# Kernel tuning notes

Hardware: AMD Instinct MI355X
Metric: run time of the kernel (lower is better)

## Reference

```python
import jax, jax.numpy as jnp
import numpy as np

B = 1024
D = 128  # in_out_dim


def _lin(k, i, o):
    return jax.random.normal(k, (i, o), jnp.float32) / np.sqrt(i)


def setup_inputs() -> dict:
    key = jax.random.key(0)
    ks = jax.random.split(key, 24)
    inp = {
        'pseudo_t': jax.random.uniform(ks[0], (), jnp.float32),
        'x': jax.random.normal(ks[1], (B, D), jnp.float32),
        'g_x': jax.random.normal(ks[2], (B, 1), jnp.float32),
        'p': jax.random.uniform(ks[3], (B, 1), jnp.float32),
        # GRN encoder: 128->1024->960->896 (Tanh), decoder 896->128
        'gw0': _lin(ks[4], 128, 1024), 'gb0': jnp.zeros((1024,), jnp.float32),
        'gw1': _lin(ks[5], 1024, 960), 'gb1': jnp.zeros((960,), jnp.float32),
        'gw2': _lin(ks[6], 960, 896), 'gb2': jnp.zeros((896,), jnp.float32),
        'gdw': _lin(ks[7], 896, 128), 'gdb': jnp.zeros((128,), jnp.float32),
        # BRD encoder: 129->512->448 (Tanh), decoder 448->1
        'bw0': _lin(ks[8], 129, 512), 'bb0': jnp.zeros((512,), jnp.float32),
        'bw1': _lin(ks[9], 512, 448), 'bb1': jnp.zeros((448,), jnp.float32),
        'bdw': _lin(ks[10], 448, 1), 'bdb': jnp.zeros((1,), jnp.float32),
    }
    return inp


def reference(pseudo_t, x, g_x, p, gw0, gb0, gw1, gb1, gw2, gb2, gdw, gdb,
              bw0, bb0, bw1, bb1, bdw, bdb):
    bsz = x.shape[0]
    x_gene = x[:, :-1]                       # [B, D-1]
    s = jnp.full((bsz, 1), pseudo_t, x.dtype)

    def grn(state):                          # [..., D] -> [..., D]
        h = jnp.tanh(state @ gw0 + gb0)
        h = jnp.tanh(h @ gw1 + gb1)
        h = jnp.tanh(h @ gw2 + gb2)
        return h @ gdw + gdb

    dx_dt = grn(jnp.concatenate([s, x_gene], axis=1))   # [B, D]

    # BRD growth function g(x, t)
    st = jnp.concatenate([s, x], axis=1)                # [B, D+1]
    e = jnp.tanh(st @ bw0 + bb0)
    e = jnp.tanh(e @ bw1 + bb1)
    g = e @ bdw + bdb                                   # [B, 1]

    # trace of d(dx_dt[:, :D-1]) / d(x_gene), per sample (CNF divergence)
    s_scalar = jnp.reshape(pseudo_t, (1,)).astype(x.dtype)

    def f_single(xg_i):                                 # [D-1] -> [D]
        return grn(jnp.concatenate([s_scalar, xg_i]))

    jac = jax.vmap(jax.jacfwd(f_single))(x_gene)        # [B, D, D-1]
    tr = jnp.trace(jac[:, :D - 1, :], axis1=1, axis2=2) # [B]

    dp_dt = g - p * tr[:, None]                         # [B, 1]
    return (dx_dt, g, dp_dt)
```

## Files before the change

### kernel.cpp

```cpp
#include <hip/hip_runtime.h>


typedef __bf16 bf16;
typedef __bf16 bf16x8 __attribute__((ext_vector_type(8)));
typedef float floatx4 __attribute__((ext_vector_type(4)));

#if defined(__has_builtin)
#if __has_builtin(__builtin_amdgcn_global_load_lds)
#define HAVE_GLL 1
#endif
#endif

typedef __attribute__((address_space(3))) char lds_char_t;
typedef __attribute__((address_space(1))) const char gbl_char_t;

__device__ inline void async_load16(const void* gp, void* lp) {
#ifdef HAVE_GLL
  __builtin_amdgcn_global_load_lds((gbl_char_t*)gp, (lds_char_t*)lp, 16, 0, 0);
#else
  *(bf16x8*)lp = *(const bf16x8*)gp;
#endif
}

__device__ inline void stage_async(const bf16* src, long row0, int ld, int kc,
                                   bf16* dst, int wid, int sr8, int cph) {
#pragma unroll
  for (int t = 0; t < 4; ++t) {
    const int r = (wid * 4 + t) * 8 + sr8;
    const int csrc = (cph - r) & 7;
    async_load16(src + (row0 + r) * (size_t)ld + kc + csrc * 8,
                 dst + r * 64 + cph * 8);
  }
}

__device__ inline void mfma_block(const bf16* As, const bf16* Bs,
                                  floatx4 (&acc)[4][4], int wm, int wn,
                                  int l16, int quad) {
#pragma unroll
  for (int ks = 0; ks < 2; ++ks) {
    bf16x8 af[4], bfv[4];
#pragma unroll
    for (int mt = 0; mt < 4; ++mt) {
      const int r = wm * 64 + mt * 16 + l16;
      const int c = (ks * 4 + quad + r) & 7;
      af[mt] = *(const bf16x8*)(As + r * 64 + c * 8);
    }
#pragma unroll
    for (int nt = 0; nt < 4; ++nt) {
      const int r = wn * 64 + nt * 16 + l16;
      const int c = (ks * 4 + quad + r) & 7;
      bfv[nt] = *(const bf16x8*)(Bs + r * 64 + c * 8);
    }
#pragma unroll
    for (int mt = 0; mt < 4; ++mt)
#pragma unroll
      for (int nt = 0; nt < 4; ++nt)
        acc[mt][nt] = __builtin_amdgcn_mfma_f32_16x16x32_bf16(af[mt], bfv[nt], acc[mt][nt], 0, 0, 0);
  }
}

__device__ inline void g0_body(bf16* G0, const bf16* gw0b, const bf16* d0b,
                               int i0, int ch, int b, int tid) {
  const int nb = ((b >> 9) << 3) + (b & 7);
  const int inner = (b >> 3) & 63;
  if (nb >= ch) return;
  const int e = inner * 256 + tid;
  const int d = e >> 7;
  const int j = (e & 127) << 3;
  const int ig = i0 + nb;
  const int wsel = (d + 1 < 128) ? d + 1 : 127;
  bf16x8 gv = *(const bf16x8*)(gw0b + wsel * 1024 + j);
  bf16x8 dv = *(const bf16x8*)(d0b + (size_t)ig * 1024 + j);
  bf16x8 v;
#pragma unroll
  for (int k = 0; k < 8; ++k) v[k] = (bf16)((float)gv[k] * (float)dv[k]);
  *(bf16x8*)(G0 + ((size_t)nb * 128 + d) * 1024 + j) = v;
}

struct T8 {
  const bf16* A;
  const bf16* Bm;
  const bf16* sc;
  bf16* Upr;
  const float* gdw;
  float* tr;
  int i0, NT, ch, nTiles;
  int chn, i0n;
  bf16* G0;
  const bf16* gw0b;
  const bf16* d0b;
};

__device__ __forceinline__ void gemm256(const bf16* Aop, const bf16* Bop,
                                        int m0, int n0, int NT, char* lds,
                                        floatx4 (&acc)[8][4]) {
  const int tid = threadIdx.x;
  const int wid = tid >> 6, lane = tid & 63;
  const int wm = wid & 1, wn = wid >> 1;
  const int quad = lane >> 4, l16 = lane & 15;

  const int sr = tid >> 2;
  const int sg = tid & 3;
  const int csrc = (sg - (sr >> 1)) & 3;
  const bf16* aSrc = Aop + (size_t)(m0 + sr) * 1024 + csrc * 8;
  const bf16* bSrc = Bop + (size_t)(n0 + sr) * 1024 + csrc * 8;

  const int rA = wm * 128 + l16;
  const int rB = wn * 64 + l16;
  const int aOff = rA * 64 + ((quad + (rA >> 1)) & 3) * 16;
  const int bOff = rB * 64 + ((quad + (rB >> 1)) & 3) * 16;

#define STAGE4(hh)                                                             \
  {                                                                            \
    char* db = lds + ((hh) & 3) * 32768;                                       \
    const int kce = (hh) * 32;                                                 \
    async_load16(aSrc + kce, db + tid * 16);                                   \
    async_load16(aSrc + 131072 + kce, db + 8192 + tid * 16);                   \
    async_load16(bSrc + kce, db + 16384 + tid * 16);                           \
    async_load16(bSrc + 131072 + kce, db + 24576 + tid * 16);                  \
  }

#define HALF_COMPUTE(HB)                                                       \
  {                                                                            \
    const char* hb_ = (const char*)(HB);                                       \
    bf16x8 af[8], bv[4];                                                       \
    _Pragma("unroll")                                                          \
    for (int nf = 0; nf < 4; ++nf)                                             \
      bv[nf] = *(const bf16x8*)(hb_ + 16384 + bOff + nf * 1024);               \
    _Pragma("unroll")                                                          \
    for (int mf = 0; mf < 8; ++mf)                                             \
      af[mf] = *(const bf16x8*)(hb_ + aOff + mf * 1024);                       \
    _Pragma("unroll")                                                          \
    for (int mf = 0; mf < 8; ++mf)                                             \
      _Pragma("unroll")                                                        \
      for (int nf = 0; nf < 4; ++nf)                                           \
        acc[mf][nf] = __builtin_amdgcn_mfma_f32_16x16x32_bf16(                 \
            af[mf], bv[nf], acc[mf][nf], 0, 0, 0);                             \
  }

#define VMW(N) asm volatile("s_waitcnt vmcnt(" #N ")" ::: "memory")
#define BARRIER()                                                              \
  asm volatile("s_barrier" ::: "memory");                                      \
  __builtin_amdgcn_sched_barrier(0)

  STAGE4(0);
  STAGE4(1);
  VMW(4);
  BARRIER();

#pragma unroll 2
  for (int t = 0; t < NT; ++t) {
    const int h0 = 2 * t;
    const bool more = (t + 1 < NT);

    if (more) STAGE4(h0 + 2);
    HALF_COMPUTE(lds + (h0 & 3) * 32768);
    if (more) VMW(4); else VMW(0);
    BARRIER();

    if (more) STAGE4(h0 + 3);
    HALF_COMPUTE(lds + ((h0 + 1) & 3) * 32768);
    if (more) {
      VMW(4);
      BARRIER();
    }
  }
#undef STAGE4
#undef HALF_COMPUTE
#undef VMW
#undef BARRIER
}

__global__ __launch_bounds__(512, 2) void kt8_b1(T8 p) {
  extern __shared__ __align__(16) char lds[];
  const int bid = blockIdx.x;
  const int nt  = ((bid >> 4) << 3) | (bid & 7);
  const int mtp = (bid >> 3) & 1;
  if (nt >= p.nTiles) return;

  const int tid = threadIdx.x;
  const int wid = tid >> 6, lane = tid & 63;
  const int wm = wid & 1, wn = wid >> 1;
  const int quad = lane >> 4, l16 = lane & 15;
  const long nLim = (long)p.ch * 128;

#pragma unroll 1
  for (int q = 0; q < 2; ++q) {
    const int mt = mtp * 2 + q;
    floatx4 acc[8][4];
#pragma unroll
    for (int a = 0; a < 8; ++a)
#pragma unroll
      for (int b = 0; b < 4; ++b)
#pragma unroll
        for (int r = 0; r < 4; ++r) acc[a][b][r] = 0.0f;

    gemm256(p.A, p.Bm, mt * 256, nt * 256, p.NT, lds, acc);

    const int mb = mt * 256 + wm * 128;
#pragma unroll
    for (int nf = 0; nf < 4; ++nf) {
      const long n = (long)nt * 256 + wn * 64 + nf * 16 + l16;
      if (n < nLim) {
        const int ig = p.i0 + (int)(n >> 7);
        const bf16* dp = p.sc + (size_t)ig * 960;
        bf16* urow = p.Upr + (size_t)n * 1024;
#pragma unroll
        for (int mf = 0; mf < 8; ++mf) {
          const int mg = mb + mf * 16 + quad * 4;
          if (mg < 960) {
            union { bf16 h[4]; uint2 u; } o;
#pragma unroll
            for (int r = 0; r < 4; ++r)
              o.h[r] = (bf16)(acc[mf][nf][r] * (float)dp[mg + r]);
            *(uint2*)(urow + mg) = o.u;
          }
        }
      }
    }
  }
}

__global__ __launch_bounds__(512, 2) void kt8_b2(T8 p) {
  extern __shared__ __align__(16) char lds[];
  const int bid = blockIdx.x;
  const int nt  = ((bid >> 4) << 3) | (bid & 7);
  const int mtp = (bid >> 3) & 1;
  const int tid = threadIdx.x;

  if (nt < p.nTiles) {
    const int wid = tid >> 6, lane = tid & 63;
    const int wm = wid & 1, wn = wid >> 1;
    const int quad = lane >> 4, l16 = lane & 15;
    const long nLim = (long)p.ch * 128;

    float s = 0.0f;
#pragma unroll 1
    for (int q = 0; q < 2; ++q) {
      const int mt = mtp * 2 + q;
      floatx4 acc[8][4];
#pragma unroll
      for (int a = 0; a < 8; ++a)
#pragma unroll
        for (int b = 0; b < 4; ++b)
#pragma unroll
          for (int r = 0; r < 4; ++r) acc[a][b][r] = 0.0f;

      gemm256(p.A, p.Bm, mt * 256, nt * 256, p.NT, lds, acc);

      const int mb = mt * 256 + wm * 128;
#pragma unroll
      for (int nf = 0; nf < 4; ++nf) {
        const long n = (long)nt * 256 + wn * 64 + nf * 16 + l16;
        const int d = (int)(n & 127);
        if (n < nLim && d < 127) {
          const int ig = p.i0 + (int)(n >> 7);
          const bf16* dp = p.sc + (size_t)ig * 896;
#pragma unroll
          for (int mf = 0; mf < 8; ++mf) {
            const int mg = mb + mf * 16 + quad * 4;
            if (mg < 896) {
#pragma unroll
              for (int r = 0; r < 4; ++r) {
                const float w = (float)dp[mg + r] * p.gdw[(mg + r) * 128 + d];
                s += acc[mf][nf][r] * w;
              }
            }
          }
        }
      }
    }
#pragma unroll
    for (int off = 1; off < 64; off <<= 1) s += __shfl_xor(s, off, 64);
    float* red = (float*)lds;
    if (lane == 0) red[wid] = s;
    __syncthreads();
    const int igA = p.i0 + nt * 2;
    if (tid == 0)
      atomicAdd(p.tr + igA, red[0] + red[1] + red[2] + red[3]);
    if (tid == 256 && nt * 2 + 1 < p.ch)
      atomicAdd(p.tr + igA + 1, red[4] + red[5] + red[6] + red[7]);
  }

  if (p.chn > 0) {
    const size_t V = (size_t)p.chn * 16384;
    for (size_t v = (size_t)blockIdx.x * 512 + tid; v < V;
         v += (size_t)gridDim.x * 512) {
      const int j = ((int)(v & 127)) << 3;
      const size_t rest = v >> 7;
      const int d = (int)(rest & 127);
      const int nb = (int)(rest >> 7);
      const int wsel = (d + 1 < 128) ? d + 1 : 127;
      bf16x8 gv = *(const bf16x8*)(p.gw0b + wsel * 1024 + j);
      bf16x8 dv = *(const bf16x8*)(p.d0b + (size_t)(p.i0n + nb) * 1024 + j);
      bf16x8 o;
#pragma unroll
      for (int k = 0; k < 8; ++k) o[k] = (bf16)((float)gv[k] * (float)dv[k]);
      *(bf16x8*)(p.G0 + ((size_t)nb * 128 + d) * 1024 + j) = o;
    }
  }
}

struct FArgs {
  const bf16* A; int lda;
  const bf16* Bt; int ldb;
  const float* bias;
  bf16* C; int ldc;
  bf16* D; int ldd;
  float* outF; int ldo;
  int K; int realN; int gridX;
};

template <int ACT>
__device__ inline void fwd_body(const FArgs& p, int bx, bf16* As, bf16* Bs) {
  const int tid  = threadIdx.x;
  const int wid  = tid >> 6, lane = tid & 63;
  const int wm   = wid & 1, wn = wid >> 1;
  const int quad = lane >> 4, l16 = lane & 15;
  const int sr8  = lane >> 3, cph = lane & 7;
  const int m0   = (bx % p.gridX) * 128;
  const int bn0  = (bx / p.gridX) * 128;

  floatx4 acc[4][4];
#pragma unroll
  for (int a = 0; a < 4; ++a)
#pragma unroll
    for (int b = 0; b < 4; ++b)
#pragma unroll
      for (int r = 0; r < 4; ++r) acc[a][b][r] = 0.0f;

  for (int kc = 0; kc < p.K; kc += 64) {
    stage_async(p.A, m0, p.lda, kc, As, wid, sr8, cph);
    stage_async(p.Bt, bn0, p.ldb, kc, Bs, wid, sr8, cph);
    __syncthreads();
    mfma_block(As, Bs, acc, wm, wn, l16, quad);
    __syncthreads();
  }

#pragma unroll
  for (int nt = 0; nt < 4; ++nt) {
    const int ng = bn0 + wn * 64 + nt * 16 + l16;
    const float bv = (ng < p.realN) ? p.bias[ng] : 0.0f;
#pragma unroll
    for (int mt = 0; mt < 4; ++mt)
#pragma unroll
      for (int r = 0; r < 4; ++r) {
        const int i = m0 + wm * 64 + mt * 16 + quad * 4 + r;
        const float v = acc[mt][nt][r] + bv;
        if (ACT) {
          const float t = tanhf(v);
          p.C[(size_t)i * p.ldc + ng] = (ng < p.realN) ? (bf16)t : (bf16)0.0f;
          if (p.D && ng < p.realN)
            p.D[(size_t)i * p.ldd + ng] = (bf16)(1.0f - t * t);
        } else if (ng < p.realN) {
          p.outF[(size_t)i * p.ldo + ng] = v;
        }
      }
  }
}

__global__ __launch_bounds__(256) void kt_fwd2(FArgs a, int na, FArgs b) {
  __shared__ __align__(16) bf16 As[8192];
  __shared__ __align__(16) bf16 Bs[8192];
  const int bx = blockIdx.x;
  if (bx < na) fwd_body<1>(a, bx, As, Bs);
  else         fwd_body<1>(b, bx - na, As, Bs);
}

__global__ __launch_bounds__(256) void kt_l2g0(FArgs a, int na, bf16* G0,
                                               const bf16* gw0b, const bf16* d0b,
                                               int i0, int ch) {
  __shared__ __align__(16) bf16 As[8192];
  __shared__ __align__(16) bf16 Bs[8192];
  const int bx = blockIdx.x;
  if (bx < na) fwd_body<1>(a, bx, As, Bs);
  else         g0_body(G0, gw0b, d0b, i0, ch, bx - na, threadIdx.x);
}

__global__ __launch_bounds__(256) void kt_dxgdot(FArgs a, int na,
                                                 const bf16* e1b, const float* bdw,
                                                 const float* bdb, float* gf,
                                                 float* gout) {
  __shared__ __align__(16) bf16 As[8192];
  __shared__ __align__(16) bf16 Bs[8192];
  const int bx = blockIdx.x;
  if (bx < na) { fwd_body<0>(a, bx, As, Bs); return; }
  const int i = (bx - na) * 4 + (threadIdx.x >> 6);
  const int lane = threadIdx.x & 63;
  float s = 0.0f;
  for (int k = lane; k < 448; k += 64) s += (float)e1b[(size_t)i * 512 + k] * bdw[k];
#pragma unroll
  for (int off = 32; off > 0; off >>= 1) s += __shfl_down(s, off, 64);
  if (lane == 0) {
    const float v = s + bdb[0];
    gf[i] = v;
    gout[i] = v;
  }
}

struct PArgs {
  const float *gw0, *gw1, *gw2, *gdw, *bw0, *bw1, *pt, *x;
  bf16 *gw0b, *gw0t, *gw1t, *gw2t, *gdwt, *bw0t, *bw1t, *Xg, *Xb;
};

__device__ inline void tpose_tile(bf16* dst, const float* src, int R, int C,
                                  int ldd, int tile, int tilesX, float* tl,
                                  int tid) {
  const int r0 = (tile % tilesX) * 64;
  const int c0 = (tile / tilesX) * 64;
  const int tx = tid & 63, ty0 = tid >> 6;
#pragma unroll
  for (int i = 0; i < 16; ++i) {
    const int ty = ty0 + i * 4;
    const int r = r0 + ty, c = c0 + tx;
    tl[ty * 65 + tx] = (r < R && c < C) ? src[(size_t)r * C + c] : 0.0f;
  }
  __syncthreads();
#pragma unroll
  for (int i = 0; i < 16; ++i) {
    const int ty = ty0 + i * 4;
    dst[(size_t)(c0 + ty) * ldd + r0 + tx] = (bf16)tl[tx * 65 + ty];
  }
}

__global__ __launch_bounds__(256) void kt_prep(PArgs p) {
  __shared__ float tl[64 * 65];
  int b = blockIdx.x;
  const int t = threadIdx.x;
  if (b < 512) { p.gw0b[b * 256 + t] = (bf16)p.gw0[b * 256 + t]; return; }
  b -= 512;
  if (b < 768) {
    const int idx = b * 256 + t;
    const int i = idx / 192, c = idx % 192;
    const float s = p.pt[0];
    float vb;
    if (c == 0) vb = s;
    else if (c <= 128) vb = p.x[i * 128 + c - 1];
    else vb = 0.0f;
    p.Xb[i * 192 + c] = (bf16)vb;
    if (c < 128) p.Xg[i * 128 + c] = (bf16)((c == 0) ? s : p.x[i * 128 + c - 1]);
    return;
  }
  b -= 768;
  if (b < 32)  { tpose_tile(p.gw0t, p.gw0, 128, 1024, 128, b, 2, tl, t);  return; }
  b -= 32;
  if (b < 256) { tpose_tile(p.gw1t, p.gw1, 1024, 960, 1024, b, 16, tl, t); return; }
  b -= 256;
  if (b < 256) { tpose_tile(p.gw2t, p.gw2, 960, 896, 1024, b, 16, tl, t); return; }
  b -= 256;
  if (b < 32)  { tpose_tile(p.gdwt, p.gdw, 896, 128, 1024, b, 16, tl, t); return; }
  b -= 32;
  if (b < 24)  { tpose_tile(p.bw0t, p.bw0, 129, 512, 192, b, 3, tl, t);  return; }
  b -= 24;
  if (b < 64)  { tpose_tile(p.bw1t, p.bw1, 512, 448, 512, b, 8, tl, t);  return; }
}

__global__ __launch_bounds__(256) void kt_fin(const float* gf, const float* tr,
                                              const float* pp, float* dp) {
  const int i = blockIdx.x * 256 + threadIdx.x;
  if (i < 1024) dp[i] = gf[i] - pp[i] * tr[i];
}

extern "C" void kernel_launch(void* const* d_in, const int* in_sizes, int n_in,
                              void* d_out, int out_size, void* d_ws, size_t ws_size,
                              hipStream_t stream) {
  const float* pt  = (const float*)d_in[0];
  const float* x   = (const float*)d_in[1];
  const float* pp  = (const float*)d_in[3];
  const float* gw0 = (const float*)d_in[4];
  const float* gb0 = (const float*)d_in[5];
  const float* gw1 = (const float*)d_in[6];
  const float* gb1 = (const float*)d_in[7];
  const float* gw2 = (const float*)d_in[8];
  const float* gb2 = (const float*)d_in[9];
  const float* gdw = (const float*)d_in[10];
  const float* gdb = (const float*)d_in[11];
  const float* bw0 = (const float*)d_in[12];
  const float* bb0 = (const float*)d_in[13];
  const float* bw1 = (const float*)d_in[14];
  const float* bb1 = (const float*)d_in[15];
  const float* bdw = (const float*)d_in[16];
  const float* bdb = (const float*)d_in[17];
  float* out = (float*)d_out;

  static bool s_attr = false;
  if (!s_attr) {
    hipFuncSetAttribute((const void*)kt8_b1,
                        hipFuncAttributeMaxDynamicSharedMemorySize, 131072);
    hipFuncSetAttribute((const void*)kt8_b2,
                        hipFuncAttributeMaxDynamicSharedMemorySize, 131072);
    s_attr = true;
  }

  char* w = (char*)d_ws;
  size_t used = 0;
  auto alloc = [&](size_t nbytes) -> void* {
    void* r = w + used;
    used += (nbytes + 255) & ~(size_t)255;
    return r;
  };
  bf16* gw0b = (bf16*)alloc((size_t)128 * 1024 * 2);
  bf16* gw0t = (bf16*)alloc((size_t)1024 * 128 * 2);
  bf16* gw1t = (bf16*)alloc((size_t)1024 * 1024 * 2);
  bf16* gw2t = (bf16*)alloc((size_t)1024 * 1024 * 2);
  bf16* gdwt = (bf16*)alloc((size_t)128 * 1024 * 2);
  bf16* bw0t = (bf16*)alloc((size_t)512 * 192 * 2);
  bf16* bw1t = (bf16*)alloc((size_t)512 * 512 * 2);
  bf16* Xg   = (bf16*)alloc((size_t)1024 * 128 * 2);
  bf16* Xb   = (bf16*)alloc((size_t)1024 * 192 * 2);
  bf16* h0b  = (bf16*)alloc((size_t)1024 * 1024 * 2);
  bf16* h1b  = (bf16*)alloc((size_t)1024 * 1024 * 2);
  bf16* h2b  = (bf16*)alloc((size_t)1024 * 1024 * 2);
  bf16* e0b  = (bf16*)alloc((size_t)1024 * 512 * 2);
  bf16* e1b  = (bf16*)alloc((size_t)1024 * 512 * 2);
  bf16* d0b  = (bf16*)alloc((size_t)1024 * 1024 * 2);
  bf16* d1b  = (bf16*)alloc((size_t)1024 * 960 * 2);
  bf16* d2b  = (bf16*)alloc((size_t)1024 * 896 * 2);
  float* gf  = (float*)alloc(1024 * 4);
  float* tr  = (float*)alloc(1024 * 4);

  const size_t perSample = (size_t)128 * 1024 * 2;
  size_t avail = (ws_size > used) ? ws_size - used : 0;
  int CH = (int)(avail / (2 * perSample));
  if (CH > 256) CH = 256;
  if (CH >= 2) CH &= ~1;
  if (CH < 1) CH = 1;
  bf16* G0  = (bf16*)alloc((size_t)CH * perSample);
  bf16* Upr = (bf16*)(w + used);

  hipMemsetAsync(tr, 0, 1024 * 4, stream);

  {
    PArgs a{gw0, gw1, gw2, gdw, bw0, bw1, pt, x,
            gw0b, gw0t, gw1t, gw2t, gdwt, bw0t, bw1t, Xg, Xb};
    kt_prep<<<dim3(1944), 256, 0, stream>>>(a);
  }

  {
    FArgs a{}; a.A = Xg; a.lda = 128; a.Bt = gw0t; a.ldb = 128; a.bias = gb0;
    a.C = h0b; a.ldc = 1024; a.D = d0b; a.ldd = 1024; a.K = 128; a.realN = 1024;
    a.gridX = 8;
    FArgs b{}; b.A = Xb; b.lda = 192; b.Bt = bw0t; b.ldb = 192; b.bias = bb0;
    b.C = e0b; b.ldc = 512; b.K = 192; b.realN = 512; b.gridX = 8;
    kt_fwd2<<<dim3(96), 256, 0, stream>>>(a, 64, b);
  }
  {
    FArgs a{}; a.A = h0b; a.lda = 1024; a.Bt = gw1t; a.ldb = 1024; a.bias = gb1;
    a.C = h1b; a.ldc = 1024; a.D = d1b; a.ldd = 960; a.K = 1024; a.realN = 960;
    a.gridX = 8;
    FArgs b{}; b.A = e0b; b.lda = 512; b.Bt = bw1t; b.ldb = 512; b.bias = bb1;
    b.C = e1b; b.ldc = 512; b.K = 512; b.realN = 448; b.gridX = 8;
    kt_fwd2<<<dim3(96), 256, 0, stream>>>(a, 64, b);
  }
  const int ch0  = (1024 < CH) ? 1024 : CH;
  const int ch08 = (ch0 + 7) & ~7;
  {
    FArgs a{}; a.A = h1b; a.lda = 1024; a.Bt = gw2t; a.ldb = 1024; a.bias = gb2;
    a.C = h2b; a.ldc = 1024; a.D = d2b; a.ldd = 896; a.K = 1024; a.realN = 896;
    a.gridX = 8;
    kt_l2g0<<<dim3(56 + ch08 * 64), 256, 0, stream>>>(a, 56, G0, gw0b, d0b, 0, ch0);
  }
  {
    FArgs a{}; a.A = h2b; a.lda = 1024; a.Bt = gdwt; a.ldb = 1024; a.bias = gdb;
    a.outF = out; a.ldo = 128; a.K = 896; a.realN = 128; a.gridX = 8;
    kt_dxgdot<<<dim3(8 + 256), 256, 0, stream>>>(a, 8, e1b, bdw, bdb, gf, out + 131072);
  }

  for (int i0 = 0; i0 < 1024; i0 += CH) {
    const int ch  = (1024 - i0 < CH) ? (1024 - i0) : CH;
    const int nTiles = (ch * 128 + 255) >> 8;
    const int nT8 = (nTiles + 7) & ~7;
    {
      T8 a{}; a.A = gw1t; a.Bm = G0; a.sc = d1b; a.Upr = Upr; a.i0 = i0;
      a.NT = 16; a.ch = ch; a.nTiles = nTiles;
      kt8_b1<<<dim3(nT8 * 2), 512, 131072, stream>>>(a);
    }
    {
      const int i0n = i0 + CH;
      const int chn = (i0n < 1024) ? ((1024 - i0n < CH) ? (1024 - i0n) : CH) : 0;
      T8 a{}; a.A = gw2t; a.Bm = Upr; a.sc = d2b; a.gdw = gdw; a.tr = tr;
      a.i0 = i0; a.NT = 15; a.ch = ch; a.nTiles = nTiles;
      a.chn = chn; a.i0n = i0n; a.G0 = G0; a.gw0b = gw0b; a.d0b = d0b;
      kt8_b2<<<dim3(nT8 * 2), 512, 131072, stream>>>(a);
    }
  }

  kt_fin<<<dim3(4), 256, 0, stream>>>(gf, tr, pp, out + 132096);
}
```

Baseline: 813.3 us.

## Fuse G0 tangent construction into first Jacobian GEMM B-operand staging

Drops the materialized G0 buffer (per-sample gw0 rows scaled by tanh' of layer 0). kt8_b1 now computes the B tile on the fly while staging, multiplying gw0 rows by d0 and writing straight to LDS. The A operand still arrives through async loads. This removes the separate G0 prep work from kt_l2g0 and kt8_b2 and frees workspace so the chunk size can double. kt8_b2 is also remapped to iterate two N tiles per block over four M tiles, with batched atomics. The cost is elementwise work and register pressure inside the GEMM staging loop, plus a different wait-count schedule.

```diff
diff --git a/kernel.cpp b/kernel.cpp
--- a/kernel.cpp
+++ b/kernel.cpp
@@ -59,36 +59,22 @@
   }
 }
 
-__device__ inline void g0_body(bf16* G0, const bf16* gw0b, const bf16* d0b,
-                               int i0, int ch, int b, int tid) {
-  const int nb = ((b >> 9) << 3) + (b & 7);
-  const int inner = (b >> 3) & 63;
-  if (nb >= ch) return;
-  const int e = inner * 256 + tid;
-  const int d = e >> 7;
-  const int j = (e & 127) << 3;
-  const int ig = i0 + nb;
-  const int wsel = (d + 1 < 128) ? d + 1 : 127;
-  bf16x8 gv = *(const bf16x8*)(gw0b + wsel * 1024 + j);
-  bf16x8 dv = *(const bf16x8*)(d0b + (size_t)ig * 1024 + j);
-  bf16x8 v;
-#pragma unroll
-  for (int k = 0; k < 8; ++k) v[k] = (bf16)((float)gv[k] * (float)dv[k]);
-  *(bf16x8*)(G0 + ((size_t)nb * 128 + d) * 1024 + j) = v;
-}
-
-struct T8 {
+struct TB1 {
+  const bf16* A;
+  const bf16* w0b;
+  const bf16* d0b;
+  const bf16* sc;
+  bf16* Upr;
+  int i0, NT, ch, nTiles;
+};
+
+struct TB2 {
   const bf16* A;
   const bf16* Bm;
   const bf16* sc;
-  bf16* Upr;
   const float* gdw;
   float* tr;
   int i0, NT, ch, nTiles;
-  int chn, i0n;
-  bf16* G0;
-  const bf16* gw0b;
-  const bf16* d0b;
 };
 
 __device__ __forceinline__ void gemm256(const bf16* Aop, const bf16* Bop,
@@ -171,7 +157,96 @@
 #undef BARRIER
 }
 
-__global__ __launch_bounds__(512, 2) void kt8_b1(T8 p) {
+__device__ __forceinline__ void gemm256_b1(const bf16* Aop, const bf16* w0p,
+                                           const bf16* d0p1, const bf16* d0p2,
+                                           int m0, int NT, char* lds,
+                                           floatx4 (&acc)[8][4]) {
+  const int tid = threadIdx.x;
+  const int wid = tid >> 6, lane = tid & 63;
+  const int wm = wid & 1, wn = wid >> 1;
+  const int quad = lane >> 4, l16 = lane & 15;
+
+  const int sr = tid >> 2;
+  const int sg = tid & 3;
+  const int csrc = (sg - (sr >> 1)) & 3;
+  const bf16* aSrc = Aop + (size_t)(m0 + sr) * 1024 + csrc * 8;
+
+  const int rA = wm * 128 + l16;
+  const int rB = wn * 64 + l16;
+  const int aOff = rA * 64 + ((quad + (rA >> 1)) & 3) * 16;
+  const int bOff = rB * 64 + ((quad + (rB >> 1)) & 3) * 16;
+
+#define STAGE1(hh)                                                             \
+  {                                                                            \
+    char* db = lds + ((hh) & 3) * 32768;                                       \
+    const int kce = (hh) * 32;                                                 \
+    bf16x8 wv = *(const bf16x8*)(w0p + kce);                                   \
+    bf16x8 v1 = *(const bf16x8*)(d0p1 + kce);                                  \
+    bf16x8 v2 = *(const bf16x8*)(d0p2 + kce);                                  \
+    async_load16(aSrc + kce, db + tid * 16);                                   \
+    async_load16(aSrc + 131072 + kce, db + 8192 + tid * 16);                   \
+    bf16x8 o1, o2;                                                             \
+    _Pragma("unroll")                                                          \
+    for (int k = 0; k < 8; ++k) {                                              \
+      o1[k] = (bf16)((float)wv[k] * (float)v1[k]);                             \
+      o2[k] = (bf16)((float)wv[k] * (float)v2[k]);                             \
+    }                                                                          \
+    *(bf16x8*)(db + 16384 + tid * 16) = o1;                                    \
+    *(bf16x8*)(db + 24576 + tid * 16) = o2;                                    \
+  }
+
+#define HALF_COMPUTE(HB)                                                       \
+  {                                                                            \
+    const char* hb_ = (const char*)(HB);                                       \
+    bf16x8 af[8], bv[4];                                                       \
+    _Pragma("unroll")                                                          \
+    for (int nf = 0; nf < 4; ++nf)                                             \
+      bv[nf] = *(const bf16x8*)(hb_ + 16384 + bOff + nf * 1024);               \
+    _Pragma("unroll")                                                          \
+    for (int mf = 0; mf < 8; ++mf)                                             \
+      af[mf] = *(const bf16x8*)(hb_ + aOff + mf * 1024);                       \
+    _Pragma("unroll")                                                          \
+    for (int mf = 0; mf < 8; ++mf)                                             \
+      _Pragma("unroll")                                                        \
+      for (int nf = 0; nf < 4; ++nf)                                           \
+        acc[mf][nf] = __builtin_amdgcn_mfma_f32_16x16x32_bf16(                 \
+            af[mf], bv[nf], acc[mf][nf], 0, 0, 0);                             \
+  }
+
+#define VMW(N) asm volatile("s_waitcnt vmcnt(" #N ")" ::: "memory")
+#define BARRIER1()                                                             \
+  asm volatile("s_waitcnt lgkmcnt(0)\ns_barrier" ::: "memory");                \
+  __builtin_amdgcn_sched_barrier(0)
+
+  STAGE1(0);
+  STAGE1(1);
+  VMW(2);
+  BARRIER1();
+
+#pragma unroll 2
+  for (int t = 0; t < NT; ++t) {
+    const int h0 = 2 * t;
+    const bool more = (t + 1 < NT);
+
+    if (more) STAGE1(h0 + 2);
+    HALF_COMPUTE(lds + (h0 & 3) * 32768);
+    if (more) VMW(2); else VMW(0);
+    BARRIER1();
+
+    if (more) STAGE1(h0 + 3);
+    HALF_COMPUTE(lds + ((h0 + 1) & 3) * 32768);
+    if (more) {
+      VMW(2);
+      BARRIER1();
+    }
+  }
+#undef STAGE1
+#undef HALF_COMPUTE
+#undef VMW
+#undef BARRIER1
+}
+
+__global__ __launch_bounds__(512, 2) void kt8_b1(TB1 p) {
   extern __shared__ __align__(16) char lds[];
   const int bid = blockIdx.x;
   const int nt  = ((bid >> 4) << 3) | (bid & 7);
@@ -184,6 +259,14 @@
   const int quad = lane >> 4, l16 = lane & 15;
   const long nLim = (long)p.ch * 128;
 
+  const int sr = tid >> 2;
+  const int sg = tid & 3;
+  const int csrc = (sg - (sr >> 1)) & 3;
+  const int wsel = (sr == 127) ? 127 : sr + 1;
+  const bf16* w0p  = p.w0b + wsel * 1024 + csrc * 8;
+  const bf16* d0p1 = p.d0b + (size_t)(p.i0 + nt * 2) * 1024 + csrc * 8;
+  const bf16* d0p2 = d0p1 + 1024;
+
 #pragma unroll 1
   for (int q = 0; q < 2; ++q) {
     const int mt = mtp * 2 + q;
@@ -195,7 +278,7 @@
 #pragma unroll
         for (int r = 0; r < 4; ++r) acc[a][b][r] = 0.0f;
 
-    gemm256(p.A, p.Bm, mt * 256, nt * 256, p.NT, lds, acc);
+    gemm256_b1(p.A, w0p, d0p1, d0p2, mt * 256, p.NT, lds, acc);
 
     const int mb = mt * 256 + wm * 128;
 #pragma unroll
@@ -221,50 +304,52 @@
   }
 }
 
-__global__ __launch_bounds__(512, 2) void kt8_b2(T8 p) {
+__global__ __launch_bounds__(512, 2) void kt8_b2(TB2 p) {
   extern __shared__ __align__(16) char lds[];
   const int bid = blockIdx.x;
-  const int nt  = ((bid >> 4) << 3) | (bid & 7);
-  const int mtp = (bid >> 3) & 1;
+  const int mt  = (bid >> 3) & 3;
+  const int ntp = ((bid >> 5) << 3) | (bid & 7);
+  const int npairs = (p.nTiles + 1) >> 1;
+  if (ntp >= npairs) return;
+
   const int tid = threadIdx.x;
-
-  if (nt < p.nTiles) {
-    const int wid = tid >> 6, lane = tid & 63;
-    const int wm = wid & 1, wn = wid >> 1;
-    const int quad = lane >> 4, l16 = lane & 15;
-    const long nLim = (long)p.ch * 128;
+  const int wid = tid >> 6, lane = tid & 63;
+  const int wm = wid & 1, wn = wid >> 1;
+  const int quad = lane >> 4, l16 = lane & 15;
+  const long nLim = (long)p.ch * 128;
+  const int mb = mt * 256 + wm * 128;
+
+  float sAB[2] = {0.0f, 0.0f};
+#pragma unroll 1
+  for (int q = 0; q < 2; ++q) {
+    const int nt = ntp * 2 + q;
+    if (nt >= p.nTiles) break;
+    floatx4 acc[8][4];
+#pragma unroll
+    for (int a = 0; a < 8; ++a)
+#pragma unroll
+      for (int b = 0; b < 4; ++b)
+#pragma unroll
+        for (int r = 0; r < 4; ++r) acc[a][b][r] = 0.0f;
+
+    gemm256(p.A, p.Bm, mt * 256, nt * 256, p.NT, lds, acc);
 
     float s = 0.0f;
-#pragma unroll 1
-    for (int q = 0; q < 2; ++q) {
-      const int mt = mtp * 2 + q;
-      floatx4 acc[8][4];
-#pragma unroll
-      for (int a = 0; a < 8; ++a)
-#pragma unroll
-        for (int b = 0; b < 4; ++b)
-#pragma unroll
-          for (int r = 0; r < 4; ++r) acc[a][b][r] = 0.0f;
-
-      gemm256(p.A, p.Bm, mt * 256, nt * 256, p.NT, lds, acc);
-
-      const int mb = mt * 256 + wm * 128;
-#pragma unroll
-      for (int nf = 0; nf < 4; ++nf) {
-        const long n = (long)nt * 256 + wn * 64 + nf * 16 + l16;
-        const int d = (int)(n & 127);
-        if (n < nLim && d < 127) {
-          const int ig = p.i0 + (int)(n >> 7);
-          const bf16* dp = p.sc + (size_t)ig * 896;
-#pragma unroll
-          for (int mf = 0; mf < 8; ++mf) {
-            const int mg = mb + mf * 16 + quad * 4;
-            if (mg < 896) {
-#pragma unroll
-              for (int r = 0; r < 4; ++r) {
-                const float w = (float)dp[mg + r] * p.gdw[(mg + r) * 128 + d];
-                s += acc[mf][nf][r] * w;
-              }
+#pragma unroll
+    for (int nf = 0; nf < 4; ++nf) {
+      const long n = (long)nt * 256 + wn * 64 + nf * 16 + l16;
+      const int d = (int)(n & 127);
+      if (n < nLim && d < 127) {
+        const int ig = p.i0 + (int)(n >> 7);
+        const bf16* dp = p.sc + (size_t)ig * 896;
+#pragma unroll
+        for (int mf = 0; mf < 8; ++mf) {
+          const int mg = mb + mf * 16 + quad * 4;
+          if (mg < 896) {
+#pragma unroll
+            for (int r = 0; r < 4; ++r) {
+              const float w = (float)dp[mg + r] * p.gdw[(mg + r) * 128 + d];
+              s += acc[mf][nf][r] * w;
             }
           }
         }
@@ -272,32 +357,22 @@
     }
 #pragma unroll
     for (int off = 1; off < 64; off <<= 1) s += __shfl_xor(s, off, 64);
-    float* red = (float*)lds;
-    if (lane == 0) red[wid] = s;
-    __syncthreads();
-    const int igA = p.i0 + nt * 2;
-    if (tid == 0)
-      atomicAdd(p.tr + igA, red[0] + red[1] + red[2] + red[3]);
-    if (tid == 256 && nt * 2 + 1 < p.ch)
-      atomicAdd(p.tr + igA + 1, red[4] + red[5] + red[6] + red[7]);
-  }
-
-  if (p.chn > 0) {
-    const size_t V = (size_t)p.chn * 16384;
-    for (size_t v = (size_t)blockIdx.x * 512 + tid; v < V;
-         v += (size_t)gridDim.x * 512) {
-      const int j = ((int)(v & 127)) << 3;
-      const size_t rest = v >> 7;
-      const int d = (int)(rest & 127);
-      const int nb = (int)(rest >> 7);
-      const int wsel = (d + 1 < 128) ? d + 1 : 127;
-      bf16x8 gv = *(const bf16x8*)(p.gw0b + wsel * 1024 + j);
-      bf16x8 dv = *(const bf16x8*)(p.d0b + (size_t)(p.i0n + nb) * 1024 + j);
-      bf16x8 o;
-#pragma unroll
-      for (int k = 0; k < 8; ++k) o[k] = (bf16)((float)gv[k] * (float)dv[k]);
-      *(bf16x8*)(p.G0 + ((size_t)nb * 128 + d) * 1024 + j) = o;
-    }
+    sAB[q] = s;
+  }
+
+  float* red = (float*)lds;
+  if (lane == 0) { red[wid] = sAB[0]; red[8 + wid] = sAB[1]; }
+  __syncthreads();
+  const int ig0 = p.i0 + ntp * 4;
+  if (tid == 0) {
+    atomicAdd(p.tr + ig0, red[0] + red[1] + red[2] + red[3]);
+    if (ntp * 2 + 1 < p.nTiles)
+      atomicAdd(p.tr + ig0 + 2, red[8] + red[9] + red[10] + red[11]);
+  }
+  if (tid == 256) {
+    atomicAdd(p.tr + ig0 + 1, red[4] + red[5] + red[6] + red[7]);
+    if (ntp * 2 + 1 < p.nTiles)
+      atomicAdd(p.tr + ig0 + 3, red[12] + red[13] + red[14] + red[15]);
   }
 }
 
@@ -367,14 +442,10 @@
   else         fwd_body<1>(b, bx - na, As, Bs);
 }
 
-__global__ __launch_bounds__(256) void kt_l2g0(FArgs a, int na, bf16* G0,
-                                               const bf16* gw0b, const bf16* d0b,
-                                               int i0, int ch) {
+__global__ __launch_bounds__(256) void kt_fwd1(FArgs a) {
   __shared__ __align__(16) bf16 As[8192];
   __shared__ __align__(16) bf16 Bs[8192];
-  const int bx = blockIdx.x;
-  if (bx < na) fwd_body<1>(a, bx, As, Bs);
-  else         g0_body(G0, gw0b, d0b, i0, ch, bx - na, threadIdx.x);
+  fwd_body<1>(a, blockIdx.x, As, Bs);
 }
 
 __global__ __launch_bounds__(256) void kt_dxgdot(FArgs a, int na,
@@ -521,11 +592,10 @@
 
   const size_t perSample = (size_t)128 * 1024 * 2;
   size_t avail = (ws_size > used) ? ws_size - used : 0;
-  int CH = (int)(avail / (2 * perSample));
+  int CH = (int)(avail / perSample);
   if (CH > 256) CH = 256;
   if (CH >= 2) CH &= ~1;
   if (CH < 1) CH = 1;
-  bf16* G0  = (bf16*)alloc((size_t)CH * perSample);
   bf16* Upr = (bf16*)(w + used);
 
   hipMemsetAsync(tr, 0, 1024 * 4, stream);
@@ -552,13 +622,11 @@
     b.C = e1b; b.ldc = 512; b.K = 512; b.realN = 448; b.gridX = 8;
     kt_fwd2<<<dim3(96), 256, 0, stream>>>(a, 64, b);
   }
-  const int ch0  = (1024 < CH) ? 1024 : CH;
-  const int ch08 = (ch0 + 7) & ~7;
   {
     FArgs a{}; a.A = h1b; a.lda = 1024; a.Bt = gw2t; a.ldb = 1024; a.bias = gb2;
     a.C = h2b; a.ldc = 1024; a.D = d2b; a.ldd = 896; a.K = 1024; a.realN = 896;
     a.gridX = 8;
-    kt_l2g0<<<dim3(56 + ch08 * 64), 256, 0, stream>>>(a, 56, G0, gw0b, d0b, 0, ch0);
+    kt_fwd1<<<dim3(56), 256, 0, stream>>>(a);
   }
   {
     FArgs a{}; a.A = h2b; a.lda = 1024; a.Bt = gdwt; a.ldb = 1024; a.bias = gdb;
@@ -571,17 +639,16 @@
     const int nTiles = (ch * 128 + 255) >> 8;
     const int nT8 = (nTiles + 7) & ~7;
     {
-      T8 a{}; a.A = gw1t; a.Bm = G0; a.sc = d1b; a.Upr = Upr; a.i0 = i0;
-      a.NT = 16; a.ch = ch; a.nTiles = nTiles;
+      TB1 a{}; a.A = gw1t; a.w0b = gw0b; a.d0b = d0b; a.sc = d1b; a.Upr = Upr;
+      a.i0 = i0; a.NT = 16; a.ch = ch; a.nTiles = nTiles;
       kt8_b1<<<dim3(nT8 * 2), 512, 131072, stream>>>(a);
     }
     {
-      const int i0n = i0 + CH;
-      const int chn = (i0n < 1024) ? ((1024 - i0n < CH) ? (1024 - i0n) : CH) : 0;
-      T8 a{}; a.A = gw2t; a.Bm = Upr; a.sc = d2b; a.gdw = gdw; a.tr = tr;
+      const int npairs = (nTiles + 1) >> 1;
+      const int np8 = (npairs + 7) & ~7;
+      TB2 a{}; a.A = gw2t; a.Bm = Upr; a.sc = d2b; a.gdw = gdw; a.tr = tr;
       a.i0 = i0; a.NT = 15; a.ch = ch; a.nTiles = nTiles;
-      a.chn = chn; a.i0n = i0n; a.G0 = G0; a.gw0b = gw0b; a.d0b = d0b;
-      kt8_b2<<<dim3(nT8 * 2), 512, 131072, stream>>>(a);
+      kt8_b2<<<dim3(np8 * 4), 512, 131072, stream>>>(a);
     }
   }
 
```

Result: no change. 826.5 us (+1.6%).
